# Kernel optimization log

Measured on AMD Instinct MI355X. Metric: run time of the kernel, lower is better.

The kernel has to match this reference:

```python
import jax, jax.numpy as jnp
import numpy as np

D_MODEL = 512
N_HEADS = 8
D_KV = 64
INNER = N_HEADS * D_KV
NUM_BUCKETS = 32
MAX_DISTANCE = 128
LN_EPS = 1e-6


def _relative_position_bucket(rel, num_buckets=NUM_BUCKETS, max_distance=MAX_DISTANCE):
    # bidirectional T5 bucketing
    nb = num_buckets // 2
    buckets = (rel > 0).astype(jnp.int32) * nb
    rel = jnp.abs(rel)
    max_exact = nb // 2
    is_small = rel < max_exact
    relf = jnp.maximum(rel.astype(jnp.float32), 1.0)  # guard log(0)
    large = max_exact + (
        jnp.log(relf / max_exact) / np.log(max_distance / max_exact) * (nb - max_exact)
    ).astype(jnp.int32)
    large = jnp.minimum(large, nb - 1)
    return buckets + jnp.where(is_small, rel, large)


def t5_layer_norm(x, weight, eps=LN_EPS):
    # T5 LayerNorm: no mean subtraction, no bias
    var = jnp.mean(jnp.square(x), axis=-1, keepdims=True)
    return x * jax.lax.rsqrt(var + eps) * weight


def compute_position_bias(rel_bias_table, q_len, k_len):
    ctx = jnp.arange(q_len)[:, None]
    mem = jnp.arange(k_len)[None, :]
    buckets = _relative_position_bucket(mem - ctx)  # [q, k]
    bias = rel_bias_table[buckets]                  # [q, k, H]
    return jnp.transpose(bias, (2, 0, 1))[None]     # [1, H, q, k]


def setup_inputs() -> dict:
    key = jax.random.key(0)
    ks = jax.random.split(key, 8)
    N, S = 8, 2048
    s = 1.0 / np.sqrt(D_MODEL)
    return {
        "hidden_states": jax.random.normal(ks[0], (N, S, D_MODEL), jnp.float32),
        "ln_weight": jnp.ones((D_MODEL,), jnp.float32),
        "wq": jax.random.normal(ks[1], (D_MODEL, INNER), jnp.float32) * s,
        "wk": jax.random.normal(ks[2], (D_MODEL, INNER), jnp.float32) * s,
        "wv": jax.random.normal(ks[3], (D_MODEL, INNER), jnp.float32) * s,
        "wo": jax.random.normal(ks[4], (INNER, D_MODEL), jnp.float32) * s,
        "rel_bias_table": jax.random.normal(ks[5], (NUM_BUCKETS, N_HEADS), jnp.float32) * 0.1,
        "seq_idx2graph_idx": jax.random.randint(ks[6], (8,), 0, 8, jnp.int64) if jax.config.jax_enable_x64 else jax.random.randint(ks[6], (8,), 0, 8, jnp.int32),
    }


def reference(hidden_states, ln_weight, wq, wk, wv, wo, rel_bias_table, seq_idx2graph_idx):
    N, S, _ = hidden_states.shape
    normed = t5_layer_norm(hidden_states, ln_weight)

    # T5Attention (no 1/sqrt(d) scaling in T5)
    q = jnp.einsum("nsd,de->nse", normed, wq).reshape(N, S, N_HEADS, D_KV)
    k = jnp.einsum("nsd,de->nse", normed, wk).reshape(N, S, N_HEADS, D_KV)
    v = jnp.einsum("nsd,de->nse", normed, wv).reshape(N, S, N_HEADS, D_KV)

    position_bias = compute_position_bias(rel_bias_table, S, S)  # [1,H,S,S]
    scores = jnp.einsum("nqhd,nkhd->nhqk", q, k) + position_bias
    attn = jax.nn.softmax(scores, axis=-1)
    ctx = jnp.einsum("nhqk,nkhd->nqhd", attn, v).reshape(N, S, INNER)
    attn_out = jnp.einsum("nse,ed->nsd", ctx, wo)

    # residual (dropout is identity in eval)
    hidden = hidden_states + attn_out
    remain_node_idx = jnp.arange(seq_idx2graph_idx.shape[0])
    return hidden, position_bias, remain_node_idx
```

## Files before the change

kernel.cpp:

```cpp
#include <hip/hip_runtime.h>
#include <hip/hip_bf16.h>
#include <math.h>

typedef __bf16 bf16;
typedef bf16 bf16x8 __attribute__((ext_vector_type(8)));
typedef bf16 bf16x4 __attribute__((ext_vector_type(4)));
typedef float f32x4 __attribute__((ext_vector_type(4)));
typedef float f32x16 __attribute__((ext_vector_type(16)));

#define MFMA16(a, b, c) __builtin_amdgcn_mfma_f32_16x16x32_bf16(a, b, c, 0, 0, 0)
#define MFMA32(a, b, c) __builtin_amdgcn_mfma_f32_32x32x16_bf16(a, b, c, 0, 0, 0)
#define LOG2E 1.4426950408889634f
#define NEG_SHIFT -40.0f

__device__ inline unsigned pkbf(float a, float b) {
  union { bf16 h; unsigned short u; } ca, cb;
  ca.h = (bf16)a;
  cb.h = (bf16)b;
  return (unsigned)ca.u | ((unsigned)cb.u << 16);
}

__device__ inline float t5bias(const float* __restrict__ table, int h, int x) {
  if (x > 4094) return 0.f;
  int rel = x - 2047;
  int bucket = (rel > 0) ? 16 : 0;
  int ar = rel < 0 ? -rel : rel;
  int v;
  if (ar < 8) {
    v = ar;
  } else {
    double tt = log((double)ar / 8.0) / log(16.0) * 8.0;
    int lg = 8 + (int)tt;
    v = lg < 15 ? lg : 15;
  }
  return table[(bucket + v) * 8 + h];
}

__global__ __launch_bounds__(256) void prep_kernel(
    const float* __restrict__ hidden, const float* __restrict__ wq,
    const float* __restrict__ wk, const float* __restrict__ wv,
    const float* __restrict__ wo, const float* __restrict__ table,
    float* __restrict__ row_scale, float* __restrict__ lut,
    float4* __restrict__ lutq, float* __restrict__ out_remain,
    bf16* __restrict__ wt_qkv, bf16* __restrict__ wt_o) {
  __shared__ float tile[32][33];
  int bid = blockIdx.x;
  int t = threadIdx.x;
  if (bid < 4096) {
    int row = bid * 4 + (t >> 6);
    int lane = t & 63;
    const float4* xr = (const float4*)(hidden + (size_t)row * 512);
    float4 a = xr[lane];
    float4 b = xr[lane + 64];
    float s = a.x * a.x + a.y * a.y + a.z * a.z + a.w * a.w +
              b.x * b.x + b.y * b.y + b.z * b.z + b.w * b.w;
#pragma unroll
    for (int off = 32; off > 0; off >>= 1) s += __shfl_down(s, off, 64);
    if (lane == 0) row_scale[row] = rsqrtf(s * (1.0f / 512.0f) + 1e-6f);
  } else if (bid < 4224) {
    int i = (bid - 4096) * 256 + t;
    int h = i >> 12;
    int d = i & 4095;
    lut[(size_t)h * 4096 + d] = t5bias(table, h, d);
    if (i < 8) out_remain[i] = (float)i;
  } else if (bid < 5248) {
    int bid2 = bid - 4224;
    int mat = bid2 >> 8;
    int rem = bid2 & 255;
    int e0 = (rem & 15) * 32;
    int k0 = (rem >> 4) * 32;
    int tx = t & 31, ty = t >> 5;
    const float* W = (mat == 0) ? wq : (mat == 1) ? wk : (mat == 2) ? wv : wo;
#pragma unroll
    for (int j = 0; j < 32; j += 8)
      tile[ty + j][tx] = W[(size_t)(k0 + ty + j) * 512 + e0 + tx];
    __syncthreads();
    bf16* dst = (mat < 3) ? (wt_qkv + (size_t)mat * 512 * 512) : wt_o;
#pragma unroll
    for (int j = 0; j < 32; j += 8)
      dst[(size_t)(e0 + ty + j) * 512 + k0 + tx] = (bf16)tile[tx][ty + j];
  } else {
    int i = (bid - 5248) * 256 + t;
    int h = i >> 12;
    int d = i & 4095;
    float4 o;
    o.x = t5bias(table, h, d);
    o.y = t5bias(table, h, d + 1);
    o.z = t5bias(table, h, d + 2);
    o.w = t5bias(table, h, d + 3);
    lutq[(size_t)h * 4096 + d] = o;
  }
}

__global__ __launch_bounds__(256) void qkv_gemm(
    const float* __restrict__ hidden, const float* __restrict__ row_scale,
    const float* __restrict__ ln_w, const bf16* __restrict__ wt,
    bf16* __restrict__ qb, bf16* __restrict__ kb, bf16* __restrict__ vb) {
  __shared__ __align__(16) char smem8[20480];
  typedef bf16 row40[40];
  row40* As = (row40*)smem8;
  row40* Bs = (row40*)(smem8 + 10240);
  int t = threadIdx.x;
  int wave = t >> 6, lane = t & 63;
  int quad = lane >> 4, lc = lane & 15;
  int wm = wave >> 1, wn = wave & 1;
  int m0 = blockIdx.x * 128;
  int n0 = blockIdx.y * 128;

  f32x4 acc[4][4];
#pragma unroll
  for (int i = 0; i < 4; i++)
#pragma unroll
    for (int j = 0; j < 4; j++) acc[i][j] = (f32x4){0.f, 0.f, 0.f, 0.f};

  int sm = t >> 1;
  int sk = (t & 1) * 16;
  const float* arow = hidden + (size_t)(m0 + sm) * 512;
  float rscale = row_scale[m0 + sm];
  const bf16* brow = wt + (size_t)(n0 + sm) * 512;

  for (int kt = 0; kt < 16; ++kt) {
    int k0 = kt * 32;
    float4 a0 = *(const float4*)(arow + k0 + sk);
    float4 a1 = *(const float4*)(arow + k0 + sk + 4);
    float4 a2 = *(const float4*)(arow + k0 + sk + 8);
    float4 a3 = *(const float4*)(arow + k0 + sk + 12);
    float4 w0 = *(const float4*)(ln_w + k0 + sk);
    float4 w1 = *(const float4*)(ln_w + k0 + sk + 4);
    float4 w2 = *(const float4*)(ln_w + k0 + sk + 8);
    float4 w3 = *(const float4*)(ln_w + k0 + sk + 12);
    bf16x8 bv0 = *(const bf16x8*)(brow + k0 + sk);
    bf16x8 bv1 = *(const bf16x8*)(brow + k0 + sk + 8);
    bf16x8 av0, av1;
    av0[0] = (bf16)(a0.x * rscale * w0.x);
    av0[1] = (bf16)(a0.y * rscale * w0.y);
    av0[2] = (bf16)(a0.z * rscale * w0.z);
    av0[3] = (bf16)(a0.w * rscale * w0.w);
    av0[4] = (bf16)(a1.x * rscale * w1.x);
    av0[5] = (bf16)(a1.y * rscale * w1.y);
    av0[6] = (bf16)(a1.z * rscale * w1.z);
    av0[7] = (bf16)(a1.w * rscale * w1.w);
    av1[0] = (bf16)(a2.x * rscale * w2.x);
    av1[1] = (bf16)(a2.y * rscale * w2.y);
    av1[2] = (bf16)(a2.z * rscale * w2.z);
    av1[3] = (bf16)(a2.w * rscale * w2.w);
    av1[4] = (bf16)(a3.x * rscale * w3.x);
    av1[5] = (bf16)(a3.y * rscale * w3.y);
    av1[6] = (bf16)(a3.z * rscale * w3.z);
    av1[7] = (bf16)(a3.w * rscale * w3.w);
    __syncthreads();
    *(bf16x8*)&As[sm][sk] = av0;
    *(bf16x8*)&As[sm][sk + 8] = av1;
    *(bf16x8*)&Bs[sm][sk] = bv0;
    *(bf16x8*)&Bs[sm][sk + 8] = bv1;
    __syncthreads();
    bf16x8 af[4], bfr[4];
#pragma unroll
    for (int i = 0; i < 4; i++)
      af[i] = *(const bf16x8*)&As[wm * 64 + i * 16 + lc][quad * 8];
#pragma unroll
    for (int j = 0; j < 4; j++)
      bfr[j] = *(const bf16x8*)&Bs[wn * 64 + j * 16 + lc][quad * 8];
#pragma unroll
    for (int i = 0; i < 4; i++)
#pragma unroll
      for (int j = 0; j < 4; j++)
        acc[i][j] = MFMA16(af[i], bfr[j], acc[i][j]);
  }

  __syncthreads();
  int mat = n0 >> 9;
  int e_base = (n0 & 511) + wn * 64;
  bf16* dst0 = (mat == 0) ? qb : (mat == 1) ? kb : vb;
  int hh = e_base >> 6;
  int grow0 = m0 + wm * 64;
  int nbi = grow0 >> 11, sbase = grow0 & 2047;
  bf16* dst = dst0 + (((size_t)nbi * 8 + hh) * 2048 + sbase) * 64;
  bf16* Cw = ((bf16*)smem8) + wave * (32 * 76);
#pragma unroll
  for (int p = 0; p < 2; ++p) {
#pragma unroll
    for (int i2 = 0; i2 < 2; ++i2) {
#pragma unroll
      for (int j = 0; j < 4; ++j)
#pragma unroll
        for (int r = 0; r < 4; ++r)
          Cw[(i2 * 16 + quad * 4 + r) * 76 + j * 16 + lc] =
              (bf16)acc[2 * p + i2][j][r];
    }
#pragma unroll
    for (int c = 0; c < 4; ++c) {
      bf16x8 vch = *(const bf16x8*)&Cw[(c * 8 + (lane >> 3)) * 76 + (lane & 7) * 8];
      *(bf16x8*)(dst + (size_t)(p * 32 + c * 8 + (lane >> 3)) * 64 + (lane & 7) * 8) = vch;
    }
  }
}

__global__ __launch_bounds__(256) void vtrans_kernel(const bf16* __restrict__ vb,
                                                     bf16* __restrict__ vtb) {
  __shared__ bf16 tl[64][72];
  int bh = blockIdx.y;
  int s0 = blockIdx.x * 64;
  int t = threadIdx.x;
  int r = t >> 2, c = (t & 3) * 16;
  const bf16* src = vb + ((size_t)bh * 2048 + s0 + r) * 64 + c;
  bf16x8 a0 = *(const bf16x8*)src;
  bf16x8 a1 = *(const bf16x8*)(src + 8);
  *(bf16x8*)&tl[r][c] = a0;
  *(bf16x8*)&tl[r][c + 8] = a1;
  __syncthreads();
  bf16x8 o0, o1;
#pragma unroll
  for (int i = 0; i < 8; i++) {
    o0[i] = tl[c + i][r];
    o1[i] = tl[c + 8 + i][r];
  }
  bf16* dst = vtb + ((size_t)bh * 64 + r) * 2048 + s0 + c;
  *(bf16x8*)dst = o0;
  *(bf16x8*)(dst + 8) = o1;
}

__global__ __launch_bounds__(256, 3) void attn_bias_kernel(
    const bf16* __restrict__ qg, const bf16* __restrict__ kg,
    const bf16* __restrict__ vtg, const float4* __restrict__ lutq,
    const float* __restrict__ lutg, bf16* __restrict__ ctx,
    float* __restrict__ bias_out) {
  __shared__ bf16 Ks[64][72];
  __shared__ bf16 Vs[64][72];
  int t = threadIdx.x;

  if (blockIdx.x >= 1024) {
    size_t i = (((size_t)blockIdx.x - 1024) * 256 + t) * 4;
    int h = (int)(i >> 22);
    int q = (int)((i >> 11) & 2047);
    int k = (int)(i & 2047);
    const float* lh = lutg + (size_t)h * 4096 + (2047 - q);
    float4 v = {lh[k], lh[k + 1], lh[k + 2], lh[k + 3]};
    *(float4*)(bias_out + i) = v;
    return;
  }

  int id = blockIdx.x;
  int xcd = id & 7, slot = id >> 3;
  int bh = xcd * 8 + (slot >> 4);
  int qt = slot & 15;
  int n = bh >> 3, h = bh & 7;
  int q0 = qt * 128;

  int wave = t >> 6, lane = t & 63;
  int l31 = lane & 31, hi = lane >> 5;
  int q = q0 + wave * 32 + l31;

  const float4* bq = lutq + (size_t)h * 4096;
  int cbase = 2047 + 4 * hi - q;

  const bf16* qp = qg + ((size_t)bh * 2048 + q) * 64;
  bf16x8 Qf[4];
#pragma unroll
  for (int c = 0; c < 4; c++) Qf[c] = *(const bf16x8*)(qp + c * 16 + hi * 8);

  f32x16 O[2];
#pragma unroll
  for (int i = 0; i < 2; i++)
#pragma unroll
    for (int e = 0; e < 16; e++) O[i][e] = 0.f;
  float lsum0 = 0.f, lsum1 = 0.f;

  int srow = t >> 2, scol = (t & 3) * 16;
  const bf16* kp = kg + (size_t)bh * 2048 * 64;
  const bf16* vp = vtg + (size_t)bh * 64 * 2048;

  bf16x8 kv0 = *(const bf16x8*)(kp + (size_t)srow * 64 + scol);
  bf16x8 kv1 = *(const bf16x8*)(kp + (size_t)srow * 64 + scol + 8);
  bf16x8 vv0 = *(const bf16x8*)(vp + (size_t)srow * 2048 + scol);
  bf16x8 vv1 = *(const bf16x8*)(vp + (size_t)srow * 2048 + scol + 8);

  for (int kt = 0; kt < 32; ++kt) {
    int kr0 = kt * 64;
    __syncthreads();
    *(bf16x8*)&Ks[srow][scol] = kv0;
    *(bf16x8*)&Ks[srow][scol + 8] = kv1;
    *(bf16x8*)&Vs[srow][scol] = vv0;
    *(bf16x8*)&Vs[srow][scol + 8] = vv1;
    __syncthreads();

    f32x16 st[2];
#pragma unroll
    for (int mi = 0; mi < 2; mi++)
#pragma unroll
      for (int g = 0; g < 4; g++) {
        float4 b4 = bq[cbase + kr0 + mi * 32 + 8 * g];
        st[mi][4 * g + 0] = b4.x;
        st[mi][4 * g + 1] = b4.y;
        st[mi][4 * g + 2] = b4.z;
        st[mi][4 * g + 3] = b4.w;
      }

    if (kt + 1 < 32) {
      int kn = kr0 + 64;
      kv0 = *(const bf16x8*)(kp + (size_t)(kn + srow) * 64 + scol);
      kv1 = *(const bf16x8*)(kp + (size_t)(kn + srow) * 64 + scol + 8);
      vv0 = *(const bf16x8*)(vp + (size_t)srow * 2048 + kn + scol);
      vv1 = *(const bf16x8*)(vp + (size_t)srow * 2048 + kn + scol + 8);
    }

#pragma unroll
    for (int mi = 0; mi < 2; mi++) {
#pragma unroll
      for (int c = 0; c < 4; c++) {
        bf16x8 kf = *(const bf16x8*)&Ks[mi * 32 + l31][c * 16 + hi * 8];
        st[mi] = MFMA32(kf, Qf[c], st[mi]);
      }
      unsigned D[8], X[8];
#pragma unroll
      for (int g = 0; g < 4; g++) {
#pragma unroll
        for (int e = 0; e < 4; e++) {
          float p = __builtin_amdgcn_exp2f(fmaf(st[mi][4 * g + e], LOG2E, NEG_SHIFT));
          st[mi][4 * g + e] = p;
          if (e & 1) lsum1 += p; else lsum0 += p;
        }
        D[2 * g] = pkbf(st[mi][4 * g + 0], st[mi][4 * g + 1]);
        D[2 * g + 1] = pkbf(st[mi][4 * g + 2], st[mi][4 * g + 3]);
      }
#pragma unroll
      for (int tt = 0; tt < 8; tt++) X[tt] = __shfl_xor(D[tt], 32, 64);

#pragma unroll
      for (int kk = 0; kk < 2; kk++) {
        int kc = 2 * mi + kk;
        int b = 4 * kk;
        unsigned f0 = hi ? X[b + 2] : D[b + 0];
        unsigned f1 = hi ? X[b + 3] : D[b + 1];
        unsigned f2 = hi ? D[b + 2] : X[b + 0];
        unsigned f3 = hi ? D[b + 3] : X[b + 1];
        union { uint4 u; bf16x8 v; } cv;
        cv.u = make_uint4(f0, f1, f2, f3);
        bf16x8 pf = cv.v;
#pragma unroll
        for (int md = 0; md < 2; md++) {
          bf16x8 vf = *(const bf16x8*)&Vs[md * 32 + l31][kc * 16 + hi * 8];
          O[md] = MFMA32(vf, pf, O[md]);
        }
      }
    }
  }

  float l_run = lsum0 + lsum1;
  l_run += __shfl_xor(l_run, 32, 64);
  float inv = 1.0f / l_run;
  bf16* cp = ctx + ((size_t)n * 2048 + q) * 512 + h * 64;
#pragma unroll
  for (int md = 0; md < 2; md++)
#pragma unroll
    for (int g = 0; g < 4; g++) {
      bf16x4 o4;
#pragma unroll
      for (int e = 0; e < 4; e++) o4[e] = (bf16)(O[md][4 * g + e] * inv);
      *(bf16x4*)(cp + md * 32 + 8 * g + hi * 4) = o4;
    }
}

__global__ __launch_bounds__(256) void oproj_gemm(
    const bf16* __restrict__ ctx, const bf16* __restrict__ wt_o,
    const float* __restrict__ hidden, float* __restrict__ out) {
  __shared__ bf16 As[128][40];
  __shared__ bf16 Bs[128][40];
  int t = threadIdx.x;
  int wave = t >> 6, lane = t & 63;
  int quad = lane >> 4, lc = lane & 15;
  int wm = wave >> 1, wn = wave & 1;
  int m0 = blockIdx.x * 128;
  int n0 = blockIdx.y * 128;

  f32x4 acc[4][4];
#pragma unroll
  for (int i = 0; i < 4; i++)
#pragma unroll
    for (int j = 0; j < 4; j++) acc[i][j] = (f32x4){0.f, 0.f, 0.f, 0.f};

  int sm = t >> 1;
  int sk = (t & 1) * 16;
  const bf16* arow = ctx + (size_t)(m0 + sm) * 512;
  const bf16* brow = wt_o + (size_t)(n0 + sm) * 512;

  for (int kt = 0; kt < 16; ++kt) {
    int k0 = kt * 32;
    bf16x8 av0 = *(const bf16x8*)(arow + k0 + sk);
    bf16x8 av1 = *(const bf16x8*)(arow + k0 + sk + 8);
    bf16x8 bv0 = *(const bf16x8*)(brow + k0 + sk);
    bf16x8 bv1 = *(const bf16x8*)(brow + k0 + sk + 8);
    __syncthreads();
    *(bf16x8*)&As[sm][sk] = av0;
    *(bf16x8*)&As[sm][sk + 8] = av1;
    *(bf16x8*)&Bs[sm][sk] = bv0;
    *(bf16x8*)&Bs[sm][sk + 8] = bv1;
    __syncthreads();
    bf16x8 af[4], bfr[4];
#pragma unroll
    for (int i = 0; i < 4; i++)
      af[i] = *(const bf16x8*)&As[wm * 64 + i * 16 + lc][quad * 8];
#pragma unroll
    for (int j = 0; j < 4; j++)
      bfr[j] = *(const bf16x8*)&Bs[wn * 64 + j * 16 + lc][quad * 8];
#pragma unroll
    for (int i = 0; i < 4; i++)
#pragma unroll
      for (int j = 0; j < 4; j++)
        acc[i][j] = MFMA16(af[i], bfr[j], acc[i][j]);
  }

#pragma unroll
  for (int i = 0; i < 4; i++) {
#pragma unroll
    for (int j = 0; j < 4; j++) {
#pragma unroll
      for (int r = 0; r < 4; r++) {
        int grow = m0 + wm * 64 + i * 16 + quad * 4 + r;
        int gcol = n0 + wn * 64 + j * 16 + lc;
        size_t idx = (size_t)grow * 512 + gcol;
        out[idx] = acc[i][j][r] + hidden[idx];
      }
    }
  }
}

extern "C" void kernel_launch(void* const* d_in, const int* in_sizes, int n_in,
                              void* d_out, int out_size, void* d_ws, size_t ws_size,
                              hipStream_t stream) {
  const float* hidden = (const float*)d_in[0];
  const float* ln_w = (const float*)d_in[1];
  const float* wq = (const float*)d_in[2];
  const float* wk = (const float*)d_in[3];
  const float* wv = (const float*)d_in[4];
  const float* wo = (const float*)d_in[5];
  const float* table = (const float*)d_in[6];

  float* out_hidden = (float*)d_out;
  float* out_bias = out_hidden + (size_t)8 * 2048 * 512;
  float* out_remain = out_bias + (size_t)8 * 2048 * 2048;

  char* ws = (char*)d_ws;
  float* row_scale = (float*)(ws + 0);
  float* lut = (float*)(ws + 65536);
  float4* lutq = (float4*)(ws + 196608);
  bf16* wt_qkv = (bf16*)(ws + 720896);
  bf16* wt_o = (bf16*)(ws + 2293760);
  bf16* qb = (bf16*)(ws + 2818048);
  bf16* kb = qb + (size_t)8 * 8 * 2048 * 64;
  bf16* vtb = kb + (size_t)8 * 8 * 2048 * 64;
  bf16* vb = vtb + (size_t)8 * 8 * 2048 * 64;
  bf16* ctx = vb;

  prep_kernel<<<dim3(5376), dim3(256), 0, stream>>>(
      hidden, wq, wk, wv, wo, table, row_scale, lut, lutq, out_remain, wt_qkv, wt_o);
  qkv_gemm<<<dim3(128, 12), dim3(256), 0, stream>>>(hidden, row_scale, ln_w, wt_qkv,
                                                    qb, kb, vb);
  vtrans_kernel<<<dim3(32, 64), dim3(256), 0, stream>>>(vb, vtb);
  attn_bias_kernel<<<dim3(1024 + 32768), dim3(256), 0, stream>>>(
      qb, kb, vtb, lutq, lut, ctx, out_bias);
  oproj_gemm<<<dim3(128, 4), dim3(256), 0, stream>>>(ctx, wt_o, hidden, out_hidden);
}
```

Before: 387.7 us.

## Prenormalize to bf16, use global_load_lds in GEMMs, fuse V transpose, double attention q-tile

The layernorm is applied once in the prep kernel and written out as a bf16 normed buffer. The QKV and O-projection GEMMs then stage tiles through direct global-to-LDS loads instead of going through registers. The V transpose kernel is removed: the QKV GEMM epilogue writes V already transposed. The attention kernel now handles 256 queries per block (two 32-row sub-tiles per wave), which halves K/V tile reloads but raises register pressure under launch_bounds(256,3). The unpadded LDS layout for the direct loads may cause bank conflicts, and the transposed V stores use strided 8-byte writes.

Measured after the change: 569.6 us. 46.9% more time.

```diff
diff --git a/kernel.cpp b/kernel.cpp
--- a/kernel.cpp
+++ b/kernel.cpp
@@ -12,6 +12,12 @@
 #define MFMA32(a, b, c) __builtin_amdgcn_mfma_f32_32x32x16_bf16(a, b, c, 0, 0, 0)
 #define LOG2E 1.4426950408889634f
 #define NEG_SHIFT -40.0f
+
+__device__ __forceinline__ void glds16(const bf16* g, bf16* l) {
+  __builtin_amdgcn_global_load_lds(
+      (const __attribute__((address_space(1))) void*)g,
+      (__attribute__((address_space(3))) void*)l, 16, 0, 0);
+}
 
 __device__ inline unsigned pkbf(float a, float b) {
   union { bf16 h; unsigned short u; } ca, cb;
@@ -37,12 +43,13 @@
 }
 
 __global__ __launch_bounds__(256) void prep_kernel(
-    const float* __restrict__ hidden, const float* __restrict__ wq,
-    const float* __restrict__ wk, const float* __restrict__ wv,
-    const float* __restrict__ wo, const float* __restrict__ table,
-    float* __restrict__ row_scale, float* __restrict__ lut,
-    float4* __restrict__ lutq, float* __restrict__ out_remain,
-    bf16* __restrict__ wt_qkv, bf16* __restrict__ wt_o) {
+    const float* __restrict__ hidden, const float* __restrict__ ln_w,
+    const float* __restrict__ wq, const float* __restrict__ wk,
+    const float* __restrict__ wv, const float* __restrict__ wo,
+    const float* __restrict__ table, bf16* __restrict__ normed,
+    float* __restrict__ lut, float4* __restrict__ lutq,
+    float* __restrict__ out_remain, bf16* __restrict__ wt_qkv,
+    bf16* __restrict__ wt_o) {
   __shared__ float tile[32][33];
   int bid = blockIdx.x;
   int t = threadIdx.x;
@@ -56,7 +63,21 @@
               b.x * b.x + b.y * b.y + b.z * b.z + b.w * b.w;
 #pragma unroll
     for (int off = 32; off > 0; off >>= 1) s += __shfl_down(s, off, 64);
-    if (lane == 0) row_scale[row] = rsqrtf(s * (1.0f / 512.0f) + 1e-6f);
+    float tot = __shfl(s, 0, 64);
+    float rscale = rsqrtf(tot * (1.0f / 512.0f) + 1e-6f);
+    float4 w0 = *(const float4*)(ln_w + 4 * lane);
+    float4 w1 = *(const float4*)(ln_w + 256 + 4 * lane);
+    bf16x4 o0, o1;
+    o0[0] = (bf16)(a.x * rscale * w0.x);
+    o0[1] = (bf16)(a.y * rscale * w0.y);
+    o0[2] = (bf16)(a.z * rscale * w0.z);
+    o0[3] = (bf16)(a.w * rscale * w0.w);
+    o1[0] = (bf16)(b.x * rscale * w1.x);
+    o1[1] = (bf16)(b.y * rscale * w1.y);
+    o1[2] = (bf16)(b.z * rscale * w1.z);
+    o1[3] = (bf16)(b.w * rscale * w1.w);
+    *(bf16x4*)(normed + (size_t)row * 512 + 4 * lane) = o0;
+    *(bf16x4*)(normed + (size_t)row * 512 + 256 + 4 * lane) = o1;
   } else if (bid < 4224) {
     int i = (bid - 4096) * 256 + t;
     int h = i >> 12;
@@ -93,19 +114,16 @@
 }
 
 __global__ __launch_bounds__(256) void qkv_gemm(
-    const float* __restrict__ hidden, const float* __restrict__ row_scale,
-    const float* __restrict__ ln_w, const bf16* __restrict__ wt,
-    bf16* __restrict__ qb, bf16* __restrict__ kb, bf16* __restrict__ vb) {
-  __shared__ __align__(16) char smem8[20480];
-  typedef bf16 row40[40];
-  row40* As = (row40*)smem8;
-  row40* Bs = (row40*)(smem8 + 10240);
+    const bf16* __restrict__ normed, const bf16* __restrict__ wt,
+    bf16* __restrict__ qb, bf16* __restrict__ kb, bf16* __restrict__ vtb) {
+  __shared__ __align__(16) char smem[19456];
+  bf16* As = (bf16*)smem;
+  bf16* Bs = (bf16*)(smem + 8192);
   int t = threadIdx.x;
   int wave = t >> 6, lane = t & 63;
   int quad = lane >> 4, lc = lane & 15;
   int wm = wave >> 1, wn = wave & 1;
-  int m0 = blockIdx.x * 128;
-  int n0 = blockIdx.y * 128;
+  int m0 = blockIdx.x * 128, n0 = blockIdx.y * 128;
 
   f32x4 acc[4][4];
 #pragma unroll
@@ -113,54 +131,28 @@
 #pragma unroll
     for (int j = 0; j < 4; j++) acc[i][j] = (f32x4){0.f, 0.f, 0.f, 0.f};
 
-  int sm = t >> 1;
-  int sk = (t & 1) * 16;
-  const float* arow = hidden + (size_t)(m0 + sm) * 512;
-  float rscale = row_scale[m0 + sm];
-  const bf16* brow = wt + (size_t)(n0 + sm) * 512;
+  int rw = lane >> 2;
+  int c8 = (lane & 3) * 8;
+  const bf16* gA = normed + (size_t)(m0 + wave * 32 + rw) * 512 + c8;
+  const bf16* gB = wt + (size_t)(n0 + wave * 32 + rw) * 512 + c8;
+  bf16* lA = As + wave * 1024;
+  bf16* lB = Bs + wave * 1024;
 
   for (int kt = 0; kt < 16; ++kt) {
     int k0 = kt * 32;
-    float4 a0 = *(const float4*)(arow + k0 + sk);
-    float4 a1 = *(const float4*)(arow + k0 + sk + 4);
-    float4 a2 = *(const float4*)(arow + k0 + sk + 8);
-    float4 a3 = *(const float4*)(arow + k0 + sk + 12);
-    float4 w0 = *(const float4*)(ln_w + k0 + sk);
-    float4 w1 = *(const float4*)(ln_w + k0 + sk + 4);
-    float4 w2 = *(const float4*)(ln_w + k0 + sk + 8);
-    float4 w3 = *(const float4*)(ln_w + k0 + sk + 12);
-    bf16x8 bv0 = *(const bf16x8*)(brow + k0 + sk);
-    bf16x8 bv1 = *(const bf16x8*)(brow + k0 + sk + 8);
-    bf16x8 av0, av1;
-    av0[0] = (bf16)(a0.x * rscale * w0.x);
-    av0[1] = (bf16)(a0.y * rscale * w0.y);
-    av0[2] = (bf16)(a0.z * rscale * w0.z);
-    av0[3] = (bf16)(a0.w * rscale * w0.w);
-    av0[4] = (bf16)(a1.x * rscale * w1.x);
-    av0[5] = (bf16)(a1.y * rscale * w1.y);
-    av0[6] = (bf16)(a1.z * rscale * w1.z);
-    av0[7] = (bf16)(a1.w * rscale * w1.w);
-    av1[0] = (bf16)(a2.x * rscale * w2.x);
-    av1[1] = (bf16)(a2.y * rscale * w2.y);
-    av1[2] = (bf16)(a2.z * rscale * w2.z);
-    av1[3] = (bf16)(a2.w * rscale * w2.w);
-    av1[4] = (bf16)(a3.x * rscale * w3.x);
-    av1[5] = (bf16)(a3.y * rscale * w3.y);
-    av1[6] = (bf16)(a3.z * rscale * w3.z);
-    av1[7] = (bf16)(a3.w * rscale * w3.w);
-    __syncthreads();
-    *(bf16x8*)&As[sm][sk] = av0;
-    *(bf16x8*)&As[sm][sk + 8] = av1;
-    *(bf16x8*)&Bs[sm][sk] = bv0;
-    *(bf16x8*)&Bs[sm][sk + 8] = bv1;
+    __syncthreads();
+    glds16(gA + k0, lA);
+    glds16(gA + 16 * 512 + k0, lA + 512);
+    glds16(gB + k0, lB);
+    glds16(gB + 16 * 512 + k0, lB + 512);
     __syncthreads();
     bf16x8 af[4], bfr[4];
 #pragma unroll
     for (int i = 0; i < 4; i++)
-      af[i] = *(const bf16x8*)&As[wm * 64 + i * 16 + lc][quad * 8];
+      af[i] = *(const bf16x8*)&As[(wm * 64 + i * 16 + lc) * 32 + quad * 8];
 #pragma unroll
     for (int j = 0; j < 4; j++)
-      bfr[j] = *(const bf16x8*)&Bs[wn * 64 + j * 16 + lc][quad * 8];
+      bfr[j] = *(const bf16x8*)&Bs[(wn * 64 + j * 16 + lc) * 32 + quad * 8];
 #pragma unroll
     for (int i = 0; i < 4; i++)
 #pragma unroll
@@ -171,53 +163,48 @@
   __syncthreads();
   int mat = n0 >> 9;
   int e_base = (n0 & 511) + wn * 64;
-  bf16* dst0 = (mat == 0) ? qb : (mat == 1) ? kb : vb;
   int hh = e_base >> 6;
   int grow0 = m0 + wm * 64;
   int nbi = grow0 >> 11, sbase = grow0 & 2047;
-  bf16* dst = dst0 + (((size_t)nbi * 8 + hh) * 2048 + sbase) * 64;
-  bf16* Cw = ((bf16*)smem8) + wave * (32 * 76);
-#pragma unroll
-  for (int p = 0; p < 2; ++p) {
-#pragma unroll
-    for (int i2 = 0; i2 < 2; ++i2) {
-#pragma unroll
-      for (int j = 0; j < 4; ++j)
-#pragma unroll
-        for (int r = 0; r < 4; ++r)
-          Cw[(i2 * 16 + quad * 4 + r) * 76 + j * 16 + lc] =
-              (bf16)acc[2 * p + i2][j][r];
+
+  if (mat == 2) {
+    bf16* dv = vtb + ((size_t)(nbi * 8 + hh) * 64) * 2048;
+#pragma unroll
+    for (int i = 0; i < 4; i++) {
+      int s = sbase + i * 16 + quad * 4;
+#pragma unroll
+      for (int j = 0; j < 4; j++) {
+        int d = j * 16 + lc;
+        bf16x4 o4;
+#pragma unroll
+        for (int r = 0; r < 4; r++) o4[r] = (bf16)acc[i][j][r];
+        *(bf16x4*)(dv + (size_t)d * 2048 + s) = o4;
+      }
     }
-#pragma unroll
-    for (int c = 0; c < 4; ++c) {
-      bf16x8 vch = *(const bf16x8*)&Cw[(c * 8 + (lane >> 3)) * 76 + (lane & 7) * 8];
-      *(bf16x8*)(dst + (size_t)(p * 32 + c * 8 + (lane >> 3)) * 64 + (lane & 7) * 8) = vch;
+  } else {
+    bf16* dst0 = (mat == 0) ? qb : kb;
+    bf16* dst = dst0 + (((size_t)nbi * 8 + hh) * 2048 + sbase) * 64;
+    bf16* Cw = (bf16*)smem + wave * 2432;
+#pragma unroll
+    for (int p = 0; p < 2; ++p) {
+#pragma unroll
+      for (int i2 = 0; i2 < 2; ++i2) {
+#pragma unroll
+        for (int j = 0; j < 4; ++j)
+#pragma unroll
+          for (int r = 0; r < 4; ++r)
+            Cw[(i2 * 16 + quad * 4 + r) * 76 + j * 16 + lc] =
+                (bf16)acc[2 * p + i2][j][r];
+      }
+#pragma unroll
+      for (int c = 0; c < 4; ++c) {
+        bf16x8 vch =
+            *(const bf16x8*)&Cw[(c * 8 + (lane >> 3)) * 76 + (lane & 7) * 8];
+        *(bf16x8*)(dst + (size_t)(p * 32 + c * 8 + (lane >> 3)) * 64 +
+                   (lane & 7) * 8) = vch;
+      }
     }
   }
-}
-
-__global__ __launch_bounds__(256) void vtrans_kernel(const bf16* __restrict__ vb,
-                                                     bf16* __restrict__ vtb) {
-  __shared__ bf16 tl[64][72];
-  int bh = blockIdx.y;
-  int s0 = blockIdx.x * 64;
-  int t = threadIdx.x;
-  int r = t >> 2, c = (t & 3) * 16;
-  const bf16* src = vb + ((size_t)bh * 2048 + s0 + r) * 64 + c;
-  bf16x8 a0 = *(const bf16x8*)src;
-  bf16x8 a1 = *(const bf16x8*)(src + 8);
-  *(bf16x8*)&tl[r][c] = a0;
-  *(bf16x8*)&tl[r][c + 8] = a1;
-  __syncthreads();
-  bf16x8 o0, o1;
-#pragma unroll
-  for (int i = 0; i < 8; i++) {
-    o0[i] = tl[c + i][r];
-    o1[i] = tl[c + 8 + i][r];
-  }
-  bf16* dst = vtb + ((size_t)bh * 64 + r) * 2048 + s0 + c;
-  *(bf16x8*)dst = o0;
-  *(bf16x8*)(dst + 8) = o1;
 }
 
 __global__ __launch_bounds__(256, 3) void attn_bias_kernel(
@@ -229,8 +216,8 @@
   __shared__ bf16 Vs[64][72];
   int t = threadIdx.x;
 
-  if (blockIdx.x >= 1024) {
-    size_t i = (((size_t)blockIdx.x - 1024) * 256 + t) * 4;
+  if (blockIdx.x >= 512) {
+    size_t i = (((size_t)blockIdx.x - 512) * 256 + t) * 4;
     int h = (int)(i >> 22);
     int q = (int)((i >> 11) & 2047);
     int k = (int)(i & 2047);
@@ -242,29 +229,33 @@
 
   int id = blockIdx.x;
   int xcd = id & 7, slot = id >> 3;
-  int bh = xcd * 8 + (slot >> 4);
-  int qt = slot & 15;
+  int bh = xcd * 8 + (slot >> 3);
+  int qt = slot & 7;
   int n = bh >> 3, h = bh & 7;
-  int q0 = qt * 128;
+  int q0 = qt * 256;
 
   int wave = t >> 6, lane = t & 63;
   int l31 = lane & 31, hi = lane >> 5;
-  int q = q0 + wave * 32 + l31;
-
+  int qA = q0 + wave * 64 + l31;
   const float4* bq = lutq + (size_t)h * 4096;
-  int cbase = 2047 + 4 * hi - q;
-
-  const bf16* qp = qg + ((size_t)bh * 2048 + q) * 64;
-  bf16x8 Qf[4];
-#pragma unroll
-  for (int c = 0; c < 4; c++) Qf[c] = *(const bf16x8*)(qp + c * 16 + hi * 8);
-
-  f32x16 O[2];
-#pragma unroll
-  for (int i = 0; i < 2; i++)
-#pragma unroll
-    for (int e = 0; e < 16; e++) O[i][e] = 0.f;
-  float lsum0 = 0.f, lsum1 = 0.f;
+  int cbA = 2047 + 4 * hi - qA;
+
+  const bf16* qp = qg + ((size_t)bh * 2048 + qA) * 64;
+  bf16x8 Qf[2][4];
+#pragma unroll
+  for (int c = 0; c < 4; c++) {
+    Qf[0][c] = *(const bf16x8*)(qp + c * 16 + hi * 8);
+    Qf[1][c] = *(const bf16x8*)(qp + 32 * 64 + c * 16 + hi * 8);
+  }
+
+  f32x16 O[2][2];
+#pragma unroll
+  for (int a = 0; a < 2; a++)
+#pragma unroll
+    for (int b = 0; b < 2; b++)
+#pragma unroll
+      for (int e = 0; e < 16; e++) O[a][b][e] = 0.f;
+  float ls0[2] = {0.f, 0.f}, ls1[2] = {0.f, 0.f};
 
   int srow = t >> 2, scol = (t & 3) * 16;
   const bf16* kp = kg + (size_t)bh * 2048 * 64;
@@ -283,19 +274,6 @@
     *(bf16x8*)&Vs[srow][scol] = vv0;
     *(bf16x8*)&Vs[srow][scol + 8] = vv1;
     __syncthreads();
-
-    f32x16 st[2];
-#pragma unroll
-    for (int mi = 0; mi < 2; mi++)
-#pragma unroll
-      for (int g = 0; g < 4; g++) {
-        float4 b4 = bq[cbase + kr0 + mi * 32 + 8 * g];
-        st[mi][4 * g + 0] = b4.x;
-        st[mi][4 * g + 1] = b4.y;
-        st[mi][4 * g + 2] = b4.z;
-        st[mi][4 * g + 3] = b4.w;
-      }
-
     if (kt + 1 < 32) {
       int kn = kr0 + 64;
       kv0 = *(const bf16x8*)(kp + (size_t)(kn + srow) * 64 + scol);
@@ -305,73 +283,89 @@
     }
 
 #pragma unroll
-    for (int mi = 0; mi < 2; mi++) {
-#pragma unroll
-      for (int c = 0; c < 4; c++) {
-        bf16x8 kf = *(const bf16x8*)&Ks[mi * 32 + l31][c * 16 + hi * 8];
-        st[mi] = MFMA32(kf, Qf[c], st[mi]);
-      }
-      unsigned D[8], X[8];
+    for (int qs = 0; qs < 2; ++qs) {
+      int cb = cbA - 32 * qs + kr0;
+#pragma unroll
+      for (int mi = 0; mi < 2; mi++) {
+        f32x16 st;
+#pragma unroll
+        for (int g = 0; g < 4; g++) {
+          float4 b4 = bq[cb + mi * 32 + 8 * g];
+          st[4 * g + 0] = b4.x;
+          st[4 * g + 1] = b4.y;
+          st[4 * g + 2] = b4.z;
+          st[4 * g + 3] = b4.w;
+        }
+#pragma unroll
+        for (int c = 0; c < 4; c++) {
+          bf16x8 kf = *(const bf16x8*)&Ks[mi * 32 + l31][c * 16 + hi * 8];
+          st = MFMA32(kf, Qf[qs][c], st);
+        }
+        unsigned D[8], X[8];
+#pragma unroll
+        for (int g = 0; g < 4; g++) {
+#pragma unroll
+          for (int e = 0; e < 4; e++) {
+            float p = __builtin_amdgcn_exp2f(fmaf(st[4 * g + e], LOG2E, NEG_SHIFT));
+            st[4 * g + e] = p;
+            if (e & 1) ls1[qs] += p; else ls0[qs] += p;
+          }
+          D[2 * g] = pkbf(st[4 * g + 0], st[4 * g + 1]);
+          D[2 * g + 1] = pkbf(st[4 * g + 2], st[4 * g + 3]);
+        }
+#pragma unroll
+        for (int tt = 0; tt < 8; tt++) X[tt] = __shfl_xor(D[tt], 32, 64);
+
+#pragma unroll
+        for (int kk = 0; kk < 2; kk++) {
+          int kc = 2 * mi + kk;
+          int b = 4 * kk;
+          unsigned f0 = hi ? X[b + 2] : D[b + 0];
+          unsigned f1 = hi ? X[b + 3] : D[b + 1];
+          unsigned f2 = hi ? D[b + 2] : X[b + 0];
+          unsigned f3 = hi ? D[b + 3] : X[b + 1];
+          union { uint4 u; bf16x8 v; } cv;
+          cv.u = make_uint4(f0, f1, f2, f3);
+          bf16x8 pf = cv.v;
+#pragma unroll
+          for (int md = 0; md < 2; md++) {
+            bf16x8 vf = *(const bf16x8*)&Vs[md * 32 + l31][kc * 16 + hi * 8];
+            O[qs][md] = MFMA32(vf, pf, O[qs][md]);
+          }
+        }
+      }
+    }
+  }
+
+#pragma unroll
+  for (int qs = 0; qs < 2; ++qs) {
+    float l_run = ls0[qs] + ls1[qs];
+    l_run += __shfl_xor(l_run, 32, 64);
+    float inv = 1.0f / l_run;
+    bf16* cp = ctx + ((size_t)n * 2048 + qA + 32 * qs) * 512 + h * 64;
+#pragma unroll
+    for (int md = 0; md < 2; md++)
 #pragma unroll
       for (int g = 0; g < 4; g++) {
-#pragma unroll
-        for (int e = 0; e < 4; e++) {
-          float p = __builtin_amdgcn_exp2f(fmaf(st[mi][4 * g + e], LOG2E, NEG_SHIFT));
-          st[mi][4 * g + e] = p;
-          if (e & 1) lsum1 += p; else lsum0 += p;
-        }
-        D[2 * g] = pkbf(st[mi][4 * g + 0], st[mi][4 * g + 1]);
-        D[2 * g + 1] = pkbf(st[mi][4 * g + 2], st[mi][4 * g + 3]);
-      }
-#pragma unroll
-      for (int tt = 0; tt < 8; tt++) X[tt] = __shfl_xor(D[tt], 32, 64);
-
-#pragma unroll
-      for (int kk = 0; kk < 2; kk++) {
-        int kc = 2 * mi + kk;
-        int b = 4 * kk;
-        unsigned f0 = hi ? X[b + 2] : D[b + 0];
-        unsigned f1 = hi ? X[b + 3] : D[b + 1];
-        unsigned f2 = hi ? D[b + 2] : X[b + 0];
-        unsigned f3 = hi ? D[b + 3] : X[b + 1];
-        union { uint4 u; bf16x8 v; } cv;
-        cv.u = make_uint4(f0, f1, f2, f3);
-        bf16x8 pf = cv.v;
-#pragma unroll
-        for (int md = 0; md < 2; md++) {
-          bf16x8 vf = *(const bf16x8*)&Vs[md * 32 + l31][kc * 16 + hi * 8];
-          O[md] = MFMA32(vf, pf, O[md]);
-        }
-      }
-    }
-  }
-
-  float l_run = lsum0 + lsum1;
-  l_run += __shfl_xor(l_run, 32, 64);
-  float inv = 1.0f / l_run;
-  bf16* cp = ctx + ((size_t)n * 2048 + q) * 512 + h * 64;
-#pragma unroll
-  for (int md = 0; md < 2; md++)
-#pragma unroll
-    for (int g = 0; g < 4; g++) {
-      bf16x4 o4;
-#pragma unroll
-      for (int e = 0; e < 4; e++) o4[e] = (bf16)(O[md][4 * g + e] * inv);
-      *(bf16x4*)(cp + md * 32 + 8 * g + hi * 4) = o4;
-    }
+        bf16x4 o4;
+#pragma unroll
+        for (int e = 0; e < 4; e++) o4[e] = (bf16)(O[qs][md][4 * g + e] * inv);
+        *(bf16x4*)(cp + md * 32 + 8 * g + hi * 4) = o4;
+      }
+  }
 }
 
 __global__ __launch_bounds__(256) void oproj_gemm(
     const bf16* __restrict__ ctx, const bf16* __restrict__ wt_o,
     const float* __restrict__ hidden, float* __restrict__ out) {
-  __shared__ bf16 As[128][40];
-  __shared__ bf16 Bs[128][40];
+  __shared__ __align__(16) char smem[16384];
+  bf16* As = (bf16*)smem;
+  bf16* Bs = (bf16*)(smem + 8192);
   int t = threadIdx.x;
   int wave = t >> 6, lane = t & 63;
   int quad = lane >> 4, lc = lane & 15;
   int wm = wave >> 1, wn = wave & 1;
-  int m0 = blockIdx.x * 128;
-  int n0 = blockIdx.y * 128;
+  int m0 = blockIdx.x * 128, n0 = blockIdx.y * 128;
 
   f32x4 acc[4][4];
 #pragma unroll
@@ -379,30 +373,28 @@
 #pragma unroll
     for (int j = 0; j < 4; j++) acc[i][j] = (f32x4){0.f, 0.f, 0.f, 0.f};
 
-  int sm = t >> 1;
-  int sk = (t & 1) * 16;
-  const bf16* arow = ctx + (size_t)(m0 + sm) * 512;
-  const bf16* brow = wt_o + (size_t)(n0 + sm) * 512;
+  int rw = lane >> 2;
+  int c8 = (lane & 3) * 8;
+  const bf16* gA = ctx + (size_t)(m0 + wave * 32 + rw) * 512 + c8;
+  const bf16* gB = wt_o + (size_t)(n0 + wave * 32 + rw) * 512 + c8;
+  bf16* lA = As + wave * 1024;
+  bf16* lB = Bs + wave * 1024;
 
   for (int kt = 0; kt < 16; ++kt) {
     int k0 = kt * 32;
-    bf16x8 av0 = *(const bf16x8*)(arow + k0 + sk);
-    bf16x8 av1 = *(const bf16x8*)(arow + k0 + sk + 8);
-    bf16x8 bv0 = *(const bf16x8*)(brow + k0 + sk);
-    bf16x8 bv1 = *(const bf16x8*)(brow + k0 + sk + 8);
-    __syncthreads();
-    *(bf16x8*)&As[sm][sk] = av0;
-    *(bf16x8*)&As[sm][sk + 8] = av1;
-    *(bf16x8*)&Bs[sm][sk] = bv0;
-    *(bf16x8*)&Bs[sm][sk + 8] = bv1;
+    __syncthreads();
+    glds16(gA + k0, lA);
+    glds16(gA + 16 * 512 + k0, lA + 512);
+    glds16(gB + k0, lB);
+    glds16(gB + 16 * 512 + k0, lB + 512);
     __syncthreads();
     bf16x8 af[4], bfr[4];
 #pragma unroll
     for (int i = 0; i < 4; i++)
-      af[i] = *(const bf16x8*)&As[wm * 64 + i * 16 + lc][quad * 8];
+      af[i] = *(const bf16x8*)&As[(wm * 64 + i * 16 + lc) * 32 + quad * 8];
 #pragma unroll
     for (int j = 0; j < 4; j++)
-      bfr[j] = *(const bf16x8*)&Bs[wn * 64 + j * 16 + lc][quad * 8];
+      bfr[j] = *(const bf16x8*)&Bs[(wn * 64 + j * 16 + lc) * 32 + quad * 8];
 #pragma unroll
     for (int i = 0; i < 4; i++)
 #pragma unroll
@@ -441,23 +433,21 @@
   float* out_remain = out_bias + (size_t)8 * 2048 * 2048;
 
   char* ws = (char*)d_ws;
-  float* row_scale = (float*)(ws + 0);
-  float* lut = (float*)(ws + 65536);
-  float4* lutq = (float4*)(ws + 196608);
-  bf16* wt_qkv = (bf16*)(ws + 720896);
-  bf16* wt_o = (bf16*)(ws + 2293760);
-  bf16* qb = (bf16*)(ws + 2818048);
+  bf16* normed = (bf16*)(ws + 0);
+  float* lut = (float*)(ws + 16777216);
+  float4* lutq = (float4*)(ws + 16908288);
+  bf16* wt_qkv = (bf16*)(ws + 17432576);
+  bf16* wt_o = (bf16*)(ws + 19005440);
+  bf16* qb = (bf16*)(ws + 19529728);
   bf16* kb = qb + (size_t)8 * 8 * 2048 * 64;
   bf16* vtb = kb + (size_t)8 * 8 * 2048 * 64;
-  bf16* vb = vtb + (size_t)8 * 8 * 2048 * 64;
-  bf16* ctx = vb;
+  bf16* ctx = normed;
 
   prep_kernel<<<dim3(5376), dim3(256), 0, stream>>>(
-      hidden, wq, wk, wv, wo, table, row_scale, lut, lutq, out_remain, wt_qkv, wt_o);
-  qkv_gemm<<<dim3(128, 12), dim3(256), 0, stream>>>(hidden, row_scale, ln_w, wt_qkv,
-                                                    qb, kb, vb);
-  vtrans_kernel<<<dim3(32, 64), dim3(256), 0, stream>>>(vb, vtb);
-  attn_bias_kernel<<<dim3(1024 + 32768), dim3(256), 0, stream>>>(
+      hidden, ln_w, wq, wk, wv, wo, table, normed, lut, lutq, out_remain,
+      wt_qkv, wt_o);
+  qkv_gemm<<<dim3(128, 12), dim3(256), 0, stream>>>(normed, wt_qkv, qb, kb, vtb);
+  attn_bias_kernel<<<dim3(512 + 32768), dim3(256), 0, stream>>>(
       qb, kb, vtb, lutq, lut, ctx, out_bias);
   oproj_gemm<<<dim3(128, 4), dim3(256), 0, stream>>>(ctx, wt_o, hidden, out_hidden);
 }
```
